# Kernel optimization log

Measured on AMD Instinct MI355X. Metric: run time of the kernel, lower is better.

The kernel has to match this reference:

```python
import jax, jax.numpy as jnp
import numpy as np

MICRO_BATCHES = 4
NUM_EXPERTS = 8  # world_size=1 -> num_local_experts = 8
EPS = 1e-5


def setup_inputs() -> dict:
    key = jax.random.key(0)
    ks = jax.random.split(key, 8)
    B, S, D = 8, 2048, 1024
    E, F = NUM_EXPERTS, 4 * D
    x = jax.random.normal(ks[0], (B, S, D), dtype=jnp.float32)
    gamma = jnp.ones((D,), jnp.float32)
    beta = jnp.zeros((D,), jnp.float32)
    gate_w = jax.random.normal(ks[1], (E, D), jnp.float32) * (1.0 / np.sqrt(D))
    w1 = jax.random.normal(ks[2], (E, D, F), jnp.float32) * (1.0 / np.sqrt(D))
    b1 = jnp.zeros((E, F), jnp.float32)
    w2 = jax.random.normal(ks[3], (E, F, D), jnp.float32) * (1.0 / np.sqrt(F))
    b2 = jnp.zeros((E, D), jnp.float32)
    return {"x": x, "gamma": gamma, "beta": beta, "gate_w": gate_w,
            "w1": w1, "b1": b1, "w2": w2, "b2": b2}


def reference(x, gamma, beta, gate_w, w1, b1, w2, b2):
    B, S, D = x.shape
    E = w1.shape[0]
    # micro-batch chunking along batch dim (chunk(MICRO_BATCHES, dim=0))
    xf = x.reshape(MICRO_BATCHES, -1, D)            # [MB, T, D], T = B/MB * S
    T = xf.shape[1]
    # residual (gated_input) is the pre-LN flat input
    # moe_norm: LayerNorm over last dim, biased variance, eps=1e-5
    mu = jnp.mean(xf, axis=-1, keepdims=True)
    var = jnp.mean(jnp.square(xf - mu), axis=-1, keepdims=True)
    xn = (xf - mu) * jax.lax.rsqrt(var + EPS) * gamma + beta  # [MB, T, D]
    # gate logits + topk are computed in the source but discarded
    _logits = jnp.einsum('mtd,ed->mte', xn, gate_w)
    _ = jax.lax.top_k(_logits, 2)
    # dispatch/combine are identity for world_size=1; tokens split round-robin
    # into num_local_experts contiguous chunks per micro-batch
    tpe = T // E
    xe = xn.reshape(MICRO_BATCHES, E, tpe, D)       # [MB, E, tpe, D]
    h = jax.nn.gelu(jnp.einsum('metd,edf->metf', xe, w1) + b1[None, :, None, :],
                    approximate=False)
    y = jnp.einsum('metf,efd->metd', h, w2) + b2[None, :, None, :]
    out = xf + y.reshape(MICRO_BATCHES, T, D)       # residual add
    return out.reshape(B, S, D)
```

## Files before the change

kernel.cpp:

```cpp
#include <hip/hip_runtime.h>
#include <stdint.h>
#include <math.h>

typedef unsigned short ushort_t;
typedef __attribute__((ext_vector_type(8))) short bf16x8;
typedef __attribute__((ext_vector_type(4))) float f32x4;

__device__ __forceinline__ ushort_t f2bf(float f) {
  union { float f; unsigned u; } cv; cv.f = f;
  unsigned r = cv.u + 0x7fffu + ((cv.u >> 16) & 1u);
  return (ushort_t)(r >> 16);
}

__device__ __forceinline__ void gl_lds16(const void* g, void* l) {
  typedef __attribute__((address_space(1))) const char gchar;
  typedef __attribute__((address_space(3))) char lchar;
  __builtin_amdgcn_global_load_lds((gchar*)g, (lchar*)l, 16, 0, 0);
}

__global__ __launch_bounds__(256) void ln_kernel(const float* __restrict__ x,
                                                 const float* __restrict__ gamma,
                                                 const float* __restrict__ beta,
                                                 ushort_t* __restrict__ xn) {
  const int row = blockIdx.x;
  const int t = threadIdx.x;
  const float4 v = ((const float4*)(x + (size_t)row * 1024))[t];
  float s  = v.x + v.y + v.z + v.w;
  float ss = v.x * v.x + v.y * v.y + v.z * v.z + v.w * v.w;
#pragma unroll
  for (int o = 32; o >= 1; o >>= 1) {
    s  += __shfl_xor(s, o);
    ss += __shfl_xor(ss, o);
  }
  __shared__ float red[10];
  const int wave = t >> 6, lane = t & 63;
  if (lane == 0) { red[wave] = s; red[4 + wave] = ss; }
  __syncthreads();
  if (t == 0) {
    float S  = red[0] + red[1] + red[2] + red[3];
    float SS = red[4] + red[5] + red[6] + red[7];
    float mu  = S * (1.0f / 1024.0f);
    float var = SS * (1.0f / 1024.0f) - mu * mu;
    red[8] = mu;
    red[9] = rsqrtf(var + 1e-5f);
  }
  __syncthreads();
  const float mu = red[8], rs = red[9];
  const float4 g = ((const float4*)gamma)[t];
  const float4 b = ((const float4*)beta)[t];
  ushort4 o;
  o.x = f2bf((v.x - mu) * rs * g.x + b.x);
  o.y = f2bf((v.y - mu) * rs * g.y + b.y);
  o.z = f2bf((v.z - mu) * rs * g.z + b.z);
  o.w = f2bf((v.w - mu) * rs * g.w + b.w);
  ((ushort4*)(xn + (size_t)row * 1024))[t] = o;
}

__global__ __launch_bounds__(256) void transpose_cast(const float* __restrict__ in,
                                                      ushort_t* __restrict__ out,
                                                      int R, int C) {
  __shared__ float tile[32][33];
  const int e = blockIdx.z;
  const float* src = in + (size_t)e * R * C;
  ushort_t* dst = out + (size_t)e * R * C;
  const int c0 = blockIdx.x * 32, r0 = blockIdx.y * 32;
  const int tx = threadIdx.x, ty = threadIdx.y;
#pragma unroll
  for (int j = 0; j < 32; j += 8)
    tile[ty + j][tx] = src[(size_t)(r0 + ty + j) * C + c0 + tx];
  __syncthreads();
#pragma unroll
  for (int j = 0; j < 32; j += 8)
    dst[(size_t)(c0 + ty + j) * R + r0 + tx] = f2bf(tile[tx][ty + j]);
}

#define SLOT_BYTES 32768

#define SYNC_V(N) do { \
  asm volatile("s_waitcnt vmcnt(" #N ") lgkmcnt(0)" ::: "memory"); \
  __builtin_amdgcn_s_barrier(); \
  asm volatile("" ::: "memory"); } while (0)

__device__ __forceinline__ void stage_tile(const ushort_t* gA, const ushort_t* gB,
                                           int lda, int ldb, char* slot, int kt,
                                           int tid, int wave) {
  const int rr = tid >> 2;
  const int gs = (tid & 3) ^ (rr & 3);
  const int kc = kt + gs * 8;
  char* ldsw = slot + wave * 1024;
  gl_lds16(gA + (size_t)rr * lda + kc,         ldsw);
  gl_lds16(gA + (size_t)(rr + 128) * lda + kc, ldsw + 8192);
  gl_lds16(gB + (size_t)rr * ldb + kc,         ldsw + 16384);
  gl_lds16(gB + (size_t)(rr + 128) * ldb + kc, ldsw + 24576);
}

__device__ __forceinline__ void compute_tile(const char* slot, int a_off, int b_off,
                                             f32x4 (&acc)[8][4]) {
  const char* sa = slot + a_off;
  const char* sb = slot + b_off;
  bf16x8 a[8], b[4];
#pragma unroll
  for (int ni = 0; ni < 4; ni++) b[ni] = *(const bf16x8*)(sb + ni * 1024);
#pragma unroll
  for (int mi = 0; mi < 4; mi++) a[mi] = *(const bf16x8*)(sa + mi * 1024);
  __builtin_amdgcn_s_setprio(1);
#pragma unroll
  for (int mi = 0; mi < 4; mi++)
#pragma unroll
    for (int ni = 0; ni < 4; ni++)
      acc[mi][ni] = __builtin_amdgcn_mfma_f32_16x16x32_bf16(a[mi], b[ni], acc[mi][ni], 0, 0, 0);
  __builtin_amdgcn_s_setprio(0);
#pragma unroll
  for (int mi = 4; mi < 8; mi++) a[mi] = *(const bf16x8*)(sa + mi * 1024);
  __builtin_amdgcn_s_setprio(1);
#pragma unroll
  for (int mi = 4; mi < 8; mi++)
#pragma unroll
    for (int ni = 0; ni < 4; ni++)
      acc[mi][ni] = __builtin_amdgcn_mfma_f32_16x16x32_bf16(a[mi], b[ni], acc[mi][ni], 0, 0, 0);
  __builtin_amdgcn_s_setprio(0);
}

template <int EPI, int LDA, int LDC, int KTOT>
__global__ __launch_bounds__(512, 2) void gemm256(const ushort_t* __restrict__ A,
                                                  const ushort_t* __restrict__ Bw,
                                                  const float* __restrict__ bias,
                                                  const float* __restrict__ resid,
                                                  ushort_t* __restrict__ Hout,
                                                  float* __restrict__ Fout) {
  extern __shared__ char smem[];
  const int tid = threadIdx.x;
  const int wave = tid >> 6, lane = tid & 63;

  const int bid = blockIdx.x;
  const int c = bid & 7, l = bid >> 3;
  const int tm = c * 8 + (l & 7);
  const int tn = l >> 3;
  const int row0 = tm * 256;
  const int col0 = tn * 256;
  const int e = (row0 >> 9) & 7;

  const ushort_t* gA = A + (size_t)row0 * LDA;
  const ushort_t* gB = Bw + ((size_t)e * LDC + col0) * LDA;

  const int NT = KTOT / 32;

  const int wm = wave >> 2, wn = wave & 3;
  const int l15 = lane & 15, g = lane >> 4;
  const int sw = ((g ^ (lane & 3)) << 4);
  const int a_off = wm * 8192 + l15 * 64 + sw;
  const int b_off = 16384 + (wn >> 1) * 8192 + (wn & 1) * 4096 + l15 * 64 + sw;

  f32x4 acc[8][4] = {};

  stage_tile(gA, gB, LDA, LDA, smem + 0 * SLOT_BYTES, 0,  tid, wave);
  stage_tile(gA, gB, LDA, LDA, smem + 1 * SLOT_BYTES, 32, tid, wave);
  stage_tile(gA, gB, LDA, LDA, smem + 2 * SLOT_BYTES, 64, tid, wave);

  for (int T = 0; T < NT - 2; ++T) {
    SYNC_V(8);
    if (T + 3 < NT)
      stage_tile(gA, gB, LDA, LDA, smem + ((T + 3) & 3) * SLOT_BYTES, (T + 3) * 32, tid, wave);
    compute_tile(smem + (T & 3) * SLOT_BYTES, a_off, b_off, acc);
  }
  SYNC_V(4);
  compute_tile(smem + ((NT - 2) & 3) * SLOT_BYTES, a_off, b_off, acc);
  SYNC_V(0);
  compute_tile(smem + ((NT - 1) & 3) * SLOT_BYTES, a_off, b_off, acc);

  const int rbase = row0 + wm * 128 + g * 4;
  const int cbase = col0 + wn * 64 + l15;
  const float* bp = bias + e * LDC;
#pragma unroll
  for (int ni = 0; ni < 4; ni++) {
    const int n = cbase + ni * 16;
    const float bv = bp[n];
#pragma unroll
    for (int mi = 0; mi < 8; mi++) {
#pragma unroll
      for (int r = 0; r < 4; r++) {
        const int row = rbase + mi * 16 + r;
        float v = acc[mi][ni][r] + bv;
        if (EPI == 0) {
          float v2 = v * v;
          float cc = fmaf(0.044715f, v2, 1.0f);
          float xa = -2.3022078f * v * cc;
          float u  = exp2f(xa);
          float o  = __fdividef(v, 1.0f + u);
          Hout[(size_t)row * LDC + n] = (ushort_t)f2bf(o);
        } else {
          const size_t idx = (size_t)row * LDC + n;
          Fout[idx] = resid[idx] + v;
        }
      }
    }
  }
}

extern "C" void kernel_launch(void* const* d_in, const int* in_sizes, int n_in,
                              void* d_out, int out_size, void* d_ws, size_t ws_size,
                              hipStream_t stream) {
  const float* x     = (const float*)d_in[0];
  const float* gamma = (const float*)d_in[1];
  const float* beta  = (const float*)d_in[2];
  const float* w1    = (const float*)d_in[4];
  const float* b1    = (const float*)d_in[5];
  const float* w2    = (const float*)d_in[6];
  const float* b2    = (const float*)d_in[7];
  float* out = (float*)d_out;

  char* ws = (char*)d_ws;
  ushort_t* xn  = (ushort_t*)ws;
  ushort_t* w1t = (ushort_t*)(ws + 33554432);
  ushort_t* w2t = (ushort_t*)(ws + 33554432 + 67108864);
  ushort_t* h   = (ushort_t*)(ws + 33554432 + 2 * 67108864);

  static bool attr_done = false;
  (void)attr_done;
  hipFuncSetAttribute(reinterpret_cast<const void*>(&gemm256<0, 1024, 4096, 1024>),
                      hipFuncAttributeMaxDynamicSharedMemorySize, 131072);
  hipFuncSetAttribute(reinterpret_cast<const void*>(&gemm256<1, 4096, 1024, 4096>),
                      hipFuncAttributeMaxDynamicSharedMemorySize, 131072);

  ln_kernel<<<16384, 256, 0, stream>>>(x, gamma, beta, xn);
  transpose_cast<<<dim3(128, 32, 8), dim3(32, 8), 0, stream>>>(w1, w1t, 1024, 4096);
  transpose_cast<<<dim3(32, 128, 8), dim3(32, 8), 0, stream>>>(w2, w2t, 4096, 1024);

  gemm256<0, 1024, 4096, 1024><<<dim3(1024), 512, 131072, stream>>>(xn, w1t, b1, nullptr, h, nullptr);
  gemm256<1, 4096, 1024, 4096><<<dim3(256), 512, 131072, stream>>>(h, w2t, b2, x, nullptr, out);
}
```

Measured before the change: 472.2 us.

## Interleave split A/B staging with MFMA phases in a ping-pong GEMM main loop

The GEMM main loop now issues the A-half loads for the next stage between LDS reads of the first compute half, and the B-half loads between the two MFMA phases. Each phase is fenced by explicit barriers so that waves alternate memory and matrix work. The LDS swizzle changes to XOR on a different lane/row bit pattern, and the loop is unrolled by four with templated waitcnt values for the tail. This adds more barriers per tile, which could cost stalls, in exchange for tighter overlap and fewer LDS bank conflicts.

```diff
diff --git a/kernel.cpp b/kernel.cpp
--- a/kernel.cpp
+++ b/kernel.cpp
@@ -5,6 +5,8 @@
 typedef unsigned short ushort_t;
 typedef __attribute__((ext_vector_type(8))) short bf16x8;
 typedef __attribute__((ext_vector_type(4))) float f32x4;
+
+#define SLOT 32768
 
 __device__ __forceinline__ ushort_t f2bf(float f) {
   union { float f; unsigned u; } cv; cv.f = f;
@@ -16,6 +18,10 @@
   typedef __attribute__((address_space(1))) const char gchar;
   typedef __attribute__((address_space(3))) char lchar;
   __builtin_amdgcn_global_load_lds((gchar*)g, (lchar*)l, 16, 0, 0);
+}
+
+__device__ __forceinline__ f32x4 MFMA(bf16x8 a, bf16x8 b, f32x4 c) {
+  return __builtin_amdgcn_mfma_f32_16x16x32_bf16(a, b, c, 0, 0, 0);
 }
 
 __global__ __launch_bounds__(256) void ln_kernel(const float* __restrict__ x,
@@ -74,51 +80,60 @@
     dst[(size_t)(c0 + ty + j) * R + r0 + tx] = f2bf(tile[tx][ty + j]);
 }
 
-#define SLOT_BYTES 32768
-
-#define SYNC_V(N) do { \
-  asm volatile("s_waitcnt vmcnt(" #N ") lgkmcnt(0)" ::: "memory"); \
-  __builtin_amdgcn_s_barrier(); \
-  asm volatile("" ::: "memory"); } while (0)
-
-__device__ __forceinline__ void stage_tile(const ushort_t* gA, const ushort_t* gB,
-                                           int lda, int ldb, char* slot, int kt,
-                                           int tid, int wave) {
+
+__device__ __forceinline__ void stage_half(const ushort_t* gsrc, int lda,
+                                           char* half_base, int kt, int tid) {
   const int rr = tid >> 2;
-  const int gs = (tid & 3) ^ (rr & 3);
-  const int kc = kt + gs * 8;
-  char* ldsw = slot + wave * 1024;
-  gl_lds16(gA + (size_t)rr * lda + kc,         ldsw);
-  gl_lds16(gA + (size_t)(rr + 128) * lda + kc, ldsw + 8192);
-  gl_lds16(gB + (size_t)rr * ldb + kc,         ldsw + 16384);
-  gl_lds16(gB + (size_t)(rr + 128) * ldb + kc, ldsw + 24576);
-}
-
-__device__ __forceinline__ void compute_tile(const char* slot, int a_off, int b_off,
-                                             f32x4 (&acc)[8][4]) {
-  const char* sa = slot + a_off;
-  const char* sb = slot + b_off;
-  bf16x8 a[8], b[4];
-#pragma unroll
-  for (int ni = 0; ni < 4; ni++) b[ni] = *(const bf16x8*)(sb + ni * 1024);
-#pragma unroll
-  for (int mi = 0; mi < 4; mi++) a[mi] = *(const bf16x8*)(sa + mi * 1024);
+  const int gs = (tid & 3) ^ ((tid >> 3) & 3);
+  gl_lds16(gsrc + (size_t)rr * lda + kt + gs * 8, half_base + (tid >> 6) * 1024);
+}
+
+template <int VM, bool STG>
+__device__ __forceinline__ void tile_body(char* smem, int T,
+                                          const ushort_t* gA, const ushort_t* gB,
+                                          int lda, int a_off, int b_off, int tid,
+                                          f32x4 (&acc)[8][4]) {
+  const char* slot = smem + (T & 3) * SLOT;
+  char* nslot = smem + ((T + 3) & 3) * SLOT;
+  const int kt3 = (T + 3) * 32;
+  bf16x8 a[4], b[4];
+#pragma unroll
+  for (int ni = 0; ni < 4; ni++) b[ni] = *(const bf16x8*)(slot + b_off + ni * 1024);
+#pragma unroll
+  for (int mi = 0; mi < 4; mi++) a[mi] = *(const bf16x8*)(slot + a_off + mi * 1024);
+  if (STG) {
+    stage_half(gA, lda, nslot, kt3, tid);
+    stage_half(gA + (size_t)128 * lda, lda, nslot + 8192, kt3, tid);
+  }
+  __builtin_amdgcn_s_barrier();
+  asm volatile("s_waitcnt lgkmcnt(0)" ::: "memory");
   __builtin_amdgcn_s_setprio(1);
 #pragma unroll
   for (int mi = 0; mi < 4; mi++)
 #pragma unroll
     for (int ni = 0; ni < 4; ni++)
-      acc[mi][ni] = __builtin_amdgcn_mfma_f32_16x16x32_bf16(a[mi], b[ni], acc[mi][ni], 0, 0, 0);
+      acc[mi][ni] = MFMA(a[mi], b[ni], acc[mi][ni]);
   __builtin_amdgcn_s_setprio(0);
-#pragma unroll
-  for (int mi = 4; mi < 8; mi++) a[mi] = *(const bf16x8*)(sa + mi * 1024);
+  __builtin_amdgcn_s_barrier();
+#pragma unroll
+  for (int mi = 0; mi < 4; mi++) a[mi] = *(const bf16x8*)(slot + a_off + (mi + 4) * 1024);
+  if (STG) {
+    stage_half(gB, lda, nslot + 16384, kt3, tid);
+    stage_half(gB + (size_t)128 * lda, lda, nslot + 24576, kt3, tid);
+  }
+  if (VM == 8)      asm volatile("s_waitcnt vmcnt(8) lgkmcnt(0)" ::: "memory");
+  else if (VM == 4) asm volatile("s_waitcnt vmcnt(4) lgkmcnt(0)" ::: "memory");
+  else if (VM == 0) asm volatile("s_waitcnt vmcnt(0) lgkmcnt(0)" ::: "memory");
+  else              asm volatile("s_waitcnt lgkmcnt(0)" ::: "memory");
+  __builtin_amdgcn_s_barrier();
   __builtin_amdgcn_s_setprio(1);
 #pragma unroll
-  for (int mi = 4; mi < 8; mi++)
+  for (int mi = 0; mi < 4; mi++)
 #pragma unroll
     for (int ni = 0; ni < 4; ni++)
-      acc[mi][ni] = __builtin_amdgcn_mfma_f32_16x16x32_bf16(a[mi], b[ni], acc[mi][ni], 0, 0, 0);
+      acc[mi + 4][ni] = MFMA(a[mi], b[ni], acc[mi + 4][ni]);
   __builtin_amdgcn_s_setprio(0);
+  __builtin_amdgcn_s_barrier();
 }
 
 template <int EPI, int LDA, int LDC, int KTOT>
@@ -147,26 +162,29 @@
 
   const int wm = wave >> 2, wn = wave & 3;
   const int l15 = lane & 15, g = lane >> 4;
-  const int sw = ((g ^ (lane & 3)) << 4);
+  const int sw = ((g ^ ((lane >> 1) & 3)) << 4);
   const int a_off = wm * 8192 + l15 * 64 + sw;
   const int b_off = 16384 + (wn >> 1) * 8192 + (wn & 1) * 4096 + l15 * 64 + sw;
 
   f32x4 acc[8][4] = {};
 
-  stage_tile(gA, gB, LDA, LDA, smem + 0 * SLOT_BYTES, 0,  tid, wave);
-  stage_tile(gA, gB, LDA, LDA, smem + 1 * SLOT_BYTES, 32, tid, wave);
-  stage_tile(gA, gB, LDA, LDA, smem + 2 * SLOT_BYTES, 64, tid, wave);
-
-  for (int T = 0; T < NT - 2; ++T) {
-    SYNC_V(8);
-    if (T + 3 < NT)
-      stage_tile(gA, gB, LDA, LDA, smem + ((T + 3) & 3) * SLOT_BYTES, (T + 3) * 32, tid, wave);
-    compute_tile(smem + (T & 3) * SLOT_BYTES, a_off, b_off, acc);
-  }
-  SYNC_V(4);
-  compute_tile(smem + ((NT - 2) & 3) * SLOT_BYTES, a_off, b_off, acc);
-  SYNC_V(0);
-  compute_tile(smem + ((NT - 1) & 3) * SLOT_BYTES, a_off, b_off, acc);
+#pragma unroll
+  for (int T = 0; T < 3; ++T) {
+    char* s = smem + T * SLOT;
+    stage_half(gA, LDA, s, T * 32, tid);
+    stage_half(gA + (size_t)128 * LDA, LDA, s + 8192, T * 32, tid);
+    stage_half(gB, LDA, s + 16384, T * 32, tid);
+    stage_half(gB + (size_t)128 * LDA, LDA, s + 24576, T * 32, tid);
+  }
+  asm volatile("s_waitcnt vmcnt(8)" ::: "memory");
+  __builtin_amdgcn_s_barrier();
+
+#pragma unroll 4
+  for (int T = 0; T < NT - 3; ++T)
+    tile_body<8, true>(smem, T, gA, gB, LDA, a_off, b_off, tid, acc);
+  tile_body<4, false>(smem, NT - 3, gA, gB, LDA, a_off, b_off, tid, acc);
+  tile_body<0, false>(smem, NT - 2, gA, gB, LDA, a_off, b_off, tid, acc);
+  tile_body<-1, false>(smem, NT - 1, gA, gB, LDA, a_off, b_off, tid, acc);
 
   const int rbase = row0 + wm * 128 + g * 4;
   const int cbase = col0 + wn * 64 + l15;
@@ -215,8 +233,6 @@
   ushort_t* w2t = (ushort_t*)(ws + 33554432 + 67108864);
   ushort_t* h   = (ushort_t*)(ws + 33554432 + 2 * 67108864);
 
-  static bool attr_done = false;
-  (void)attr_done;
   hipFuncSetAttribute(reinterpret_cast<const void*>(&gemm256<0, 1024, 4096, 1024>),
                       hipFuncAttributeMaxDynamicSharedMemorySize, 131072);
   hipFuncSetAttribute(reinterpret_cast<const void*>(&gemm256<1, 4096, 1024, 4096>),
```

Result: no change. 463.8 us (-1.8%).
